# Kernel optimization log

Hardware: AMD Instinct MI355X
Metric: run time of the kernel (lower is better)

The kernel has to match this reference:

```python
import jax, jax.numpy as jnp
import numpy as np

B, T, D, H = 256, 256, 384, 64  # batch, seq (BLOCK_SIZE), D_MODEL, HEAD_SIZE


def setup_inputs() -> dict:
    key = jax.random.key(0)
    k1, k2, k3, k4 = jax.random.split(key, 4)
    x = jax.random.normal(k1, (B, T, D), dtype=jnp.float32)
    # nn.Linear(D, H, bias=False): weight [H, D]; we store transposed [D, H] for x @ W
    Wq = jax.random.normal(k2, (D, H), dtype=jnp.float32) * (1.0 / np.sqrt(D))
    Wk = jax.random.normal(k3, (D, H), dtype=jnp.float32) * (1.0 / np.sqrt(D))
    Wv = jax.random.normal(k4, (D, H), dtype=jnp.float32) * (1.0 / np.sqrt(D))
    return {"x": x, "Wq": Wq, "Wk": Wk, "Wv": Wv}


def reference(x, Wq, Wk, Wv):
    # x: [B, T, D]
    q = x @ Wq  # [B, T, H]
    k = x @ Wk  # [B, T, H]
    v = x @ Wv  # [B, T, H]
    scale = 1.0 / jnp.sqrt(jnp.asarray(k.shape[-1], dtype=x.dtype))
    wei = jnp.einsum('bth,bsh->bts', q, k) * scale  # [B, T, T]
    causal = jnp.tril(jnp.ones((x.shape[1], x.shape[1]), dtype=bool))
    wei = jnp.where(causal, wei, -jnp.inf)
    wei = jax.nn.softmax(wei, axis=-1)
    # dropout is identity in eval mode (deterministic reference)
    out = jnp.einsum('bts,bsh->bth', wei, v)  # [B, T, H]
    return out
```

## Files before the change

kernel.cpp:

```cpp
#include <hip/hip_runtime.h>

#define BATCH 256
#define TT 256
#define DD 384
#define HH 64
#define SCALE 0.125f

typedef __attribute__((ext_vector_type(8))) short short8;
typedef __attribute__((ext_vector_type(4))) float floatx4;

#define KS_STRIDE 72
#define VT_STRIDE 264
#define QS_STRIDE 72
#define PS_STRIDE 40

__device__ __forceinline__ unsigned short f2bf(float f) {
    unsigned int u = __float_as_uint(f);
    u += 0x7fffu + ((u >> 16) & 1u);
    return (unsigned short)(u >> 16);
}

__device__ __forceinline__ short8 cvt8(const float* __restrict__ p) {
    float4 f0 = *(const float4*)p;
    float4 f1 = *(const float4*)(p + 4);
    short8 r;
    r[0] = (short)f2bf(f0.x); r[1] = (short)f2bf(f0.y);
    r[2] = (short)f2bf(f0.z); r[3] = (short)f2bf(f0.w);
    r[4] = (short)f2bf(f1.x); r[5] = (short)f2bf(f1.y);
    r[6] = (short)f2bf(f1.z); r[7] = (short)f2bf(f1.w);
    return r;
}

__global__ void transpose_w_kernel(const float* __restrict__ wq,
                                   const float* __restrict__ wk,
                                   const float* __restrict__ wv,
                                   unsigned short* __restrict__ wt) {
    int idx = blockIdx.x * 256 + threadIdx.x;
    if (idx >= 3 * DD * HH) return;
    int mat = idx / (DD * HH);
    int rem = idx - mat * (DD * HH);
    int d = rem / HH;
    int h = rem - d * HH;
    const float* w = (mat == 0) ? wq : (mat == 1) ? wk : wv;
    wt[(mat * HH + h) * DD + d] = f2bf(w[d * HH + h]);
}

__global__ __launch_bounds__(512, 2)
void attn_kernel(const float* __restrict__ x,
                 const unsigned short* __restrict__ wt,
                 float* __restrict__ out) {
    __shared__ __align__(16) unsigned short Ks[TT * KS_STRIDE];
    __shared__ __align__(16) unsigned short Vt[HH * VT_STRIDE];
    __shared__ __align__(16) unsigned short Scr[8 * 32 * QS_STRIDE];

    const int b = blockIdx.x;
    const int tid = threadIdx.x;
    const int wave = tid >> 6;
    const int lane = tid & 63;
    const int quad = lane >> 4;
    const int l16 = lane & 15;

    const float* xb = x + (size_t)b * TT * DD;

    floatx4 cq[2][4] = {};
    floatx4 ck[2][4] = {};
    floatx4 cv[2][4] = {};

    for (int kk = 0; kk < DD; kk += 32) {
        short8 a[2];
        #pragma unroll
        for (int mi = 0; mi < 2; ++mi) {
            int row = 32 * wave + 16 * mi + l16;
            a[mi] = cvt8(xb + row * DD + kk + quad * 8);
        }
        #pragma unroll
        for (int nt = 0; nt < 4; ++nt) {
            int n = 16 * nt + l16;
            short8 bq = *(const short8*)(wt + (0 * HH + n) * DD + kk + quad * 8);
            short8 bk = *(const short8*)(wt + (1 * HH + n) * DD + kk + quad * 8);
            short8 bv = *(const short8*)(wt + (2 * HH + n) * DD + kk + quad * 8);
            #pragma unroll
            for (int mi = 0; mi < 2; ++mi) {
                cq[mi][nt] = __builtin_amdgcn_mfma_f32_16x16x32_bf16(a[mi], bq, cq[mi][nt], 0, 0, 0);
                ck[mi][nt] = __builtin_amdgcn_mfma_f32_16x16x32_bf16(a[mi], bk, ck[mi][nt], 0, 0, 0);
                cv[mi][nt] = __builtin_amdgcn_mfma_f32_16x16x32_bf16(a[mi], bv, cv[mi][nt], 0, 0, 0);
            }
        }
    }

    unsigned short* qscr = Scr + wave * 32 * QS_STRIDE;
    #pragma unroll
    for (int mi = 0; mi < 2; ++mi)
      #pragma unroll
      for (int nt = 0; nt < 4; ++nt)
        #pragma unroll
        for (int r = 0; r < 4; ++r) {
            int rl = 16 * mi + 4 * quad + r;
            int col = 16 * nt + l16;
            qscr[rl * QS_STRIDE + col] = f2bf(cq[mi][nt][r]);
            int row = 32 * wave + rl;
            Ks[row * KS_STRIDE + col] = f2bf(ck[mi][nt][r]);
            Vt[col * VT_STRIDE + row] = f2bf(cv[mi][nt][r]);
        }

    __syncthreads();

    short8 aq[2][2];
    #pragma unroll
    for (int mi = 0; mi < 2; ++mi)
      #pragma unroll
      for (int ks = 0; ks < 2; ++ks)
        aq[mi][ks] = *(const short8*)(qscr + (16 * mi + l16) * QS_STRIDE + 32 * ks + quad * 8);

    floatx4 o[2][4] = {};
    float m_run[2][4], l_run[2][4];
    #pragma unroll
    for (int mi = 0; mi < 2; ++mi)
      #pragma unroll
      for (int r = 0; r < 4; ++r) { m_run[mi][r] = -1e30f; l_run[mi][r] = 0.f; }

    unsigned short* ps = Scr + wave * 32 * QS_STRIDE;

    for (int c = 0; c <= wave; ++c) {
        floatx4 s[2][2] = {};
        #pragma unroll
        for (int ks = 0; ks < 2; ++ks) {
            #pragma unroll
            for (int ni = 0; ni < 2; ++ni) {
                short8 bk = *(const short8*)(Ks + (32 * c + 16 * ni + l16) * KS_STRIDE + 32 * ks + quad * 8);
                #pragma unroll
                for (int mi = 0; mi < 2; ++mi)
                    s[mi][ni] = __builtin_amdgcn_mfma_f32_16x16x32_bf16(aq[mi][ks], bk, s[mi][ni], 0, 0, 0);
            }
        }
        #pragma unroll
        for (int mi = 0; mi < 2; ++mi) {
            #pragma unroll
            for (int r = 0; r < 4; ++r) {
                int row = 32 * wave + 16 * mi + 4 * quad + r;
                float v0 = s[mi][0][r] * SCALE;
                float v1 = s[mi][1][r] * SCALE;
                int c0 = 32 * c + l16;
                if (c0 > row) v0 = -1e30f;
                if (c0 + 16 > row) v1 = -1e30f;
                float t = fmaxf(v0, v1);
                t = fmaxf(t, __shfl_xor(t, 1));
                t = fmaxf(t, __shfl_xor(t, 2));
                t = fmaxf(t, __shfl_xor(t, 4));
                t = fmaxf(t, __shfl_xor(t, 8));
                float mn = fmaxf(m_run[mi][r], t);
                float alpha = __expf(m_run[mi][r] - mn);
                float p0 = __expf(v0 - mn);
                float p1 = __expf(v1 - mn);
                float rs = p0 + p1;
                rs += __shfl_xor(rs, 1);
                rs += __shfl_xor(rs, 2);
                rs += __shfl_xor(rs, 4);
                rs += __shfl_xor(rs, 8);
                l_run[mi][r] = l_run[mi][r] * alpha + rs;
                m_run[mi][r] = mn;
                #pragma unroll
                for (int nt = 0; nt < 4; ++nt) o[mi][nt][r] *= alpha;
                int rl = 16 * mi + 4 * quad + r;
                ps[rl * PS_STRIDE + l16] = f2bf(p0);
                ps[rl * PS_STRIDE + 16 + l16] = f2bf(p1);
            }
        }
        short8 ap[2];
        #pragma unroll
        for (int mi = 0; mi < 2; ++mi)
            ap[mi] = *(const short8*)(ps + (16 * mi + l16) * PS_STRIDE + quad * 8);
        #pragma unroll
        for (int nt = 0; nt < 4; ++nt) {
            short8 bv = *(const short8*)(Vt + (16 * nt + l16) * VT_STRIDE + 32 * c + quad * 8);
            #pragma unroll
            for (int mi = 0; mi < 2; ++mi)
                o[mi][nt] = __builtin_amdgcn_mfma_f32_16x16x32_bf16(ap[mi], bv, o[mi][nt], 0, 0, 0);
        }
    }

    float* outb = out + (size_t)b * TT * HH;
    #pragma unroll
    for (int mi = 0; mi < 2; ++mi)
      #pragma unroll
      for (int nt = 0; nt < 4; ++nt)
        #pragma unroll
        for (int r = 0; r < 4; ++r) {
            int row = 32 * wave + 16 * mi + 4 * quad + r;
            outb[row * HH + 16 * nt + l16] = o[mi][nt][r] / l_run[mi][r];
        }
}

extern "C" void kernel_launch(void* const* d_in, const int* in_sizes, int n_in,
                              void* d_out, int out_size, void* d_ws, size_t ws_size,
                              hipStream_t stream) {
    const float* x  = (const float*)d_in[0];
    const float* wq = (const float*)d_in[1];
    const float* wk = (const float*)d_in[2];
    const float* wv = (const float*)d_in[3];
    unsigned short* wt = (unsigned short*)d_ws;
    float* o = (float*)d_out;

    transpose_w_kernel<<<(3 * DD * HH + 255) / 256, 256, 0, stream>>>(wq, wk, wv, wt);
    attn_kernel<<<BATCH, 512, 0, stream>>>(x, wt, o);
}
```

Before: 203.2 us.

## Split fused attention into a QKV projection kernel and a query-tiled attention kernel

The single per-batch kernel, which projected Q/K/V into LDS and then ran causal attention, is split into two kernels. A QKV kernel with 64 rows per block writes bf16 Q, K and transposed V to workspace. An attention kernel then launches 4 blocks per batch (one per 64-query tile) and reads K and V straight from global memory. This gives more blocks and better balance of the causal triangle across CUs, and frees LDS for higher occupancy. The cost is a round trip of the intermediates through global memory, one extra launch, and K/V tiles being read repeatedly without LDS staging.

```diff
diff --git a/kernel.cpp b/kernel.cpp
--- a/kernel.cpp
+++ b/kernel.cpp
@@ -8,11 +8,6 @@
 
 typedef __attribute__((ext_vector_type(8))) short short8;
 typedef __attribute__((ext_vector_type(4))) float floatx4;
-
-#define KS_STRIDE 72
-#define VT_STRIDE 264
-#define QS_STRIDE 72
-#define PS_STRIDE 40
 
 __device__ __forceinline__ unsigned short f2bf(float f) {
     unsigned int u = __float_as_uint(f);
@@ -45,150 +40,147 @@
     wt[(mat * HH + h) * DD + d] = f2bf(w[d * HH + h]);
 }
 
-__global__ __launch_bounds__(512, 2)
-void attn_kernel(const float* __restrict__ x,
-                 const unsigned short* __restrict__ wt,
-                 float* __restrict__ out) {
-    __shared__ __align__(16) unsigned short Ks[TT * KS_STRIDE];
-    __shared__ __align__(16) unsigned short Vt[HH * VT_STRIDE];
-    __shared__ __align__(16) unsigned short Scr[8 * 32 * QS_STRIDE];
-
-    const int b = blockIdx.x;
+__global__ __launch_bounds__(256, 4)
+void qkv_kernel(const float* __restrict__ x, const unsigned short* __restrict__ wt,
+                unsigned short* __restrict__ q, unsigned short* __restrict__ k,
+                unsigned short* __restrict__ vt) {
+    __shared__ __align__(16) unsigned short vts[4][64 * 24];
+
     const int tid = threadIdx.x;
     const int wave = tid >> 6;
     const int lane = tid & 63;
     const int quad = lane >> 4;
     const int l16 = lane & 15;
 
-    const float* xb = x + (size_t)b * TT * DD;
-
-    floatx4 cq[2][4] = {};
-    floatx4 ck[2][4] = {};
-    floatx4 cv[2][4] = {};
+    const int R0 = blockIdx.x * 64;
+    const int arow = R0 + 16 * wave + l16;
+
+    floatx4 c[3][4] = {};
 
     for (int kk = 0; kk < DD; kk += 32) {
-        short8 a[2];
-        #pragma unroll
-        for (int mi = 0; mi < 2; ++mi) {
-            int row = 32 * wave + 16 * mi + l16;
-            a[mi] = cvt8(xb + row * DD + kk + quad * 8);
+        short8 a = cvt8(x + (size_t)arow * DD + kk + quad * 8);
+        #pragma unroll
+        for (int mat = 0; mat < 3; ++mat)
+          #pragma unroll
+          for (int nt = 0; nt < 4; ++nt) {
+            short8 bf = *(const short8*)(wt + (size_t)(mat * HH + 16 * nt + l16) * DD + kk + quad * 8);
+            c[mat][nt] = __builtin_amdgcn_mfma_f32_16x16x32_bf16(a, bf, c[mat][nt], 0, 0, 0);
+          }
+    }
+
+    #pragma unroll
+    for (int nt = 0; nt < 4; ++nt)
+      #pragma unroll
+      for (int r = 0; r < 4; ++r) {
+        int gr = R0 + 16 * wave + 4 * quad + r;
+        q[(size_t)gr * HH + 16 * nt + l16] = f2bf(c[0][nt][r]);
+        k[(size_t)gr * HH + 16 * nt + l16] = f2bf(c[1][nt][r]);
+      }
+
+    unsigned short* tile = vts[wave];
+    #pragma unroll
+    for (int nt = 0; nt < 4; ++nt)
+      #pragma unroll
+      for (int r = 0; r < 4; ++r)
+        tile[(16 * nt + l16) * 24 + 4 * quad + r] = f2bf(c[2][nt][r]);
+
+    __syncthreads();
+
+    const int b = R0 >> 8;
+    const int tbase = (R0 & 255) + 16 * wave;
+    #pragma unroll
+    for (int p = 0; p < 2; ++p) {
+        short8 vv = *(const short8*)(tile + lane * 24 + p * 8);
+        *(short8*)(vt + (size_t)b * HH * TT + (size_t)lane * TT + tbase + p * 8) = vv;
+    }
+}
+
+__global__ __launch_bounds__(256, 4)
+void attn_kernel(const unsigned short* __restrict__ q, const unsigned short* __restrict__ k,
+                 const unsigned short* __restrict__ vt, float* __restrict__ out) {
+    __shared__ __align__(16) unsigned short ps[4][16 * 40];
+
+    const int tid = threadIdx.x;
+    const int wave = tid >> 6;
+    const int lane = tid & 63;
+    const int quad = lane >> 4;
+    const int l16 = lane & 15;
+
+    const int b = blockIdx.x >> 2;
+    const int tq = blockIdx.x & 3;
+    const int r0 = 64 * tq + 16 * wave;
+
+    const unsigned short* qb = q + (size_t)b * TT * HH;
+    const unsigned short* kb = k + (size_t)b * TT * HH;
+    const unsigned short* vb = vt + (size_t)b * HH * TT;
+
+    short8 aq[2];
+    #pragma unroll
+    for (int ks = 0; ks < 2; ++ks)
+        aq[ks] = *(const short8*)(qb + (size_t)(r0 + l16) * HH + ks * 32 + quad * 8);
+
+    floatx4 o[4] = {};
+    float m_run[4], l_run[4];
+    #pragma unroll
+    for (int r = 0; r < 4; ++r) { m_run[r] = -1e30f; l_run[r] = 0.f; }
+
+    unsigned short* psw = ps[wave];
+    const int cmax = (r0 + 15) >> 5;
+
+    for (int c = 0; c <= cmax; ++c) {
+        floatx4 s[2] = {};
+        #pragma unroll
+        for (int ks = 0; ks < 2; ++ks)
+          #pragma unroll
+          for (int ni = 0; ni < 2; ++ni) {
+            short8 bk = *(const short8*)(kb + (size_t)(32 * c + 16 * ni + l16) * HH + ks * 32 + quad * 8);
+            s[ni] = __builtin_amdgcn_mfma_f32_16x16x32_bf16(aq[ks], bk, s[ni], 0, 0, 0);
+          }
+        #pragma unroll
+        for (int r = 0; r < 4; ++r) {
+            int row = r0 + 4 * quad + r;
+            float v0 = s[0][r] * SCALE;
+            float v1 = s[1][r] * SCALE;
+            int c0 = 32 * c + l16;
+            if (c0 > row) v0 = -1e30f;
+            if (c0 + 16 > row) v1 = -1e30f;
+            float t = fmaxf(v0, v1);
+            t = fmaxf(t, __shfl_xor(t, 1));
+            t = fmaxf(t, __shfl_xor(t, 2));
+            t = fmaxf(t, __shfl_xor(t, 4));
+            t = fmaxf(t, __shfl_xor(t, 8));
+            float mn = fmaxf(m_run[r], t);
+            float alpha = __expf(m_run[r] - mn);
+            float p0 = __expf(v0 - mn);
+            float p1 = __expf(v1 - mn);
+            float rs = p0 + p1;
+            rs += __shfl_xor(rs, 1);
+            rs += __shfl_xor(rs, 2);
+            rs += __shfl_xor(rs, 4);
+            rs += __shfl_xor(rs, 8);
+            l_run[r] = l_run[r] * alpha + rs;
+            m_run[r] = mn;
+            #pragma unroll
+            for (int nt = 0; nt < 4; ++nt) o[nt][r] *= alpha;
+            psw[(4 * quad + r) * 40 + l16] = f2bf(p0);
+            psw[(4 * quad + r) * 40 + 16 + l16] = f2bf(p1);
         }
+        short8 ap = *(const short8*)(psw + l16 * 40 + quad * 8);
         #pragma unroll
         for (int nt = 0; nt < 4; ++nt) {
-            int n = 16 * nt + l16;
-            short8 bq = *(const short8*)(wt + (0 * HH + n) * DD + kk + quad * 8);
-            short8 bk = *(const short8*)(wt + (1 * HH + n) * DD + kk + quad * 8);
-            short8 bv = *(const short8*)(wt + (2 * HH + n) * DD + kk + quad * 8);
-            #pragma unroll
-            for (int mi = 0; mi < 2; ++mi) {
-                cq[mi][nt] = __builtin_amdgcn_mfma_f32_16x16x32_bf16(a[mi], bq, cq[mi][nt], 0, 0, 0);
-                ck[mi][nt] = __builtin_amdgcn_mfma_f32_16x16x32_bf16(a[mi], bk, ck[mi][nt], 0, 0, 0);
-                cv[mi][nt] = __builtin_amdgcn_mfma_f32_16x16x32_bf16(a[mi], bv, cv[mi][nt], 0, 0, 0);
-            }
+            short8 bv = *(const short8*)(vb + (size_t)(16 * nt + l16) * TT + 32 * c + quad * 8);
+            o[nt] = __builtin_amdgcn_mfma_f32_16x16x32_bf16(ap, bv, o[nt], 0, 0, 0);
         }
     }
 
-    unsigned short* qscr = Scr + wave * 32 * QS_STRIDE;
-    #pragma unroll
-    for (int mi = 0; mi < 2; ++mi)
+    float* outb = out + (size_t)b * TT * HH;
+    #pragma unroll
+    for (int nt = 0; nt < 4; ++nt)
       #pragma unroll
-      for (int nt = 0; nt < 4; ++nt)
-        #pragma unroll
-        for (int r = 0; r < 4; ++r) {
-            int rl = 16 * mi + 4 * quad + r;
-            int col = 16 * nt + l16;
-            qscr[rl * QS_STRIDE + col] = f2bf(cq[mi][nt][r]);
-            int row = 32 * wave + rl;
-            Ks[row * KS_STRIDE + col] = f2bf(ck[mi][nt][r]);
-            Vt[col * VT_STRIDE + row] = f2bf(cv[mi][nt][r]);
-        }
-
-    __syncthreads();
-
-    short8 aq[2][2];
-    #pragma unroll
-    for (int mi = 0; mi < 2; ++mi)
-      #pragma unroll
-      for (int ks = 0; ks < 2; ++ks)
-        aq[mi][ks] = *(const short8*)(qscr + (16 * mi + l16) * QS_STRIDE + 32 * ks + quad * 8);
-
-    floatx4 o[2][4] = {};
-    float m_run[2][4], l_run[2][4];
-    #pragma unroll
-    for (int mi = 0; mi < 2; ++mi)
-      #pragma unroll
-      for (int r = 0; r < 4; ++r) { m_run[mi][r] = -1e30f; l_run[mi][r] = 0.f; }
-
-    unsigned short* ps = Scr + wave * 32 * QS_STRIDE;
-
-    for (int c = 0; c <= wave; ++c) {
-        floatx4 s[2][2] = {};
-        #pragma unroll
-        for (int ks = 0; ks < 2; ++ks) {
-            #pragma unroll
-            for (int ni = 0; ni < 2; ++ni) {
-                short8 bk = *(const short8*)(Ks + (32 * c + 16 * ni + l16) * KS_STRIDE + 32 * ks + quad * 8);
-                #pragma unroll
-                for (int mi = 0; mi < 2; ++mi)
-                    s[mi][ni] = __builtin_amdgcn_mfma_f32_16x16x32_bf16(aq[mi][ks], bk, s[mi][ni], 0, 0, 0);
-            }
-        }
-        #pragma unroll
-        for (int mi = 0; mi < 2; ++mi) {
-            #pragma unroll
-            for (int r = 0; r < 4; ++r) {
-                int row = 32 * wave + 16 * mi + 4 * quad + r;
-                float v0 = s[mi][0][r] * SCALE;
-                float v1 = s[mi][1][r] * SCALE;
-                int c0 = 32 * c + l16;
-                if (c0 > row) v0 = -1e30f;
-                if (c0 + 16 > row) v1 = -1e30f;
-                float t = fmaxf(v0, v1);
-                t = fmaxf(t, __shfl_xor(t, 1));
-                t = fmaxf(t, __shfl_xor(t, 2));
-                t = fmaxf(t, __shfl_xor(t, 4));
-                t = fmaxf(t, __shfl_xor(t, 8));
-                float mn = fmaxf(m_run[mi][r], t);
-                float alpha = __expf(m_run[mi][r] - mn);
-                float p0 = __expf(v0 - mn);
-                float p1 = __expf(v1 - mn);
-                float rs = p0 + p1;
-                rs += __shfl_xor(rs, 1);
-                rs += __shfl_xor(rs, 2);
-                rs += __shfl_xor(rs, 4);
-                rs += __shfl_xor(rs, 8);
-                l_run[mi][r] = l_run[mi][r] * alpha + rs;
-                m_run[mi][r] = mn;
-                #pragma unroll
-                for (int nt = 0; nt < 4; ++nt) o[mi][nt][r] *= alpha;
-                int rl = 16 * mi + 4 * quad + r;
-                ps[rl * PS_STRIDE + l16] = f2bf(p0);
-                ps[rl * PS_STRIDE + 16 + l16] = f2bf(p1);
-            }
-        }
-        short8 ap[2];
-        #pragma unroll
-        for (int mi = 0; mi < 2; ++mi)
-            ap[mi] = *(const short8*)(ps + (16 * mi + l16) * PS_STRIDE + quad * 8);
-        #pragma unroll
-        for (int nt = 0; nt < 4; ++nt) {
-            short8 bv = *(const short8*)(Vt + (16 * nt + l16) * VT_STRIDE + 32 * c + quad * 8);
-            #pragma unroll
-            for (int mi = 0; mi < 2; ++mi)
-                o[mi][nt] = __builtin_amdgcn_mfma_f32_16x16x32_bf16(ap[mi], bv, o[mi][nt], 0, 0, 0);
-        }
-    }
-
-    float* outb = out + (size_t)b * TT * HH;
-    #pragma unroll
-    for (int mi = 0; mi < 2; ++mi)
-      #pragma unroll
-      for (int nt = 0; nt < 4; ++nt)
-        #pragma unroll
-        for (int r = 0; r < 4; ++r) {
-            int row = 32 * wave + 16 * mi + 4 * quad + r;
-            outb[row * HH + 16 * nt + l16] = o[mi][nt][r] / l_run[mi][r];
-        }
+      for (int r = 0; r < 4; ++r) {
+        int row = r0 + 4 * quad + r;
+        outb[(size_t)row * HH + 16 * nt + l16] = o[nt][r] / l_run[r];
+      }
 }
 
 extern "C" void kernel_launch(void* const* d_in, const int* in_sizes, int n_in,
@@ -198,9 +190,15 @@
     const float* wq = (const float*)d_in[1];
     const float* wk = (const float*)d_in[2];
     const float* wv = (const float*)d_in[3];
-    unsigned short* wt = (unsigned short*)d_ws;
     float* o = (float*)d_out;
 
+    const size_t QBYTES = (size_t)BATCH * TT * HH * 2;
+    unsigned short* wt  = (unsigned short*)d_ws;
+    unsigned short* qws = (unsigned short*)((char*)d_ws + 147456);
+    unsigned short* kws = (unsigned short*)((char*)d_ws + 147456 + QBYTES);
+    unsigned short* vtws= (unsigned short*)((char*)d_ws + 147456 + 2 * QBYTES);
+
     transpose_w_kernel<<<(3 * DD * HH + 255) / 256, 256, 0, stream>>>(wq, wk, wv, wt);
-    attn_kernel<<<BATCH, 512, 0, stream>>>(x, wt, o);
-}
+    qkv_kernel<<<BATCH * TT / 64, 256, 0, stream>>>(x, wt, qws, kws, vtws);
+    attn_kernel<<<BATCH * 4, 256, 0, stream>>>(qws, kws, vtws, o);
+}
```

Result: slower. 247.1 us (+21.6%).
